# Kernel tuning notes

Measured on AMD Instinct MI355X. Metric: run time of the kernel, lower is better.

The kernel has to match this reference:

```python
import jax, jax.numpy as jnp
import numpy as np

N_NODES = 100000


def gin_layer(x, src, dst, W, b):
    # GINConv with Linear nn, eps=0: Linear(x + sum_{j in N(i)} x_j)
    agg = jax.ops.segment_sum(x[src], dst, num_segments=N_NODES)  # [N, d]
    return (x + agg) @ W + b


def setup_inputs() -> dict:
    key = jax.random.key(0)
    ks = jax.random.split(key, 8)
    in_c, hid, out_c = 128, 128, 64
    x = jax.random.normal(ks[0], (N_NODES, in_c), dtype=jnp.float32)
    edge_index = jax.random.randint(ks[1], (2, 600000), 0, N_NODES, dtype=jnp.int64)
    def lin(k, fan_in, fan_out):
        bound = 1.0 / np.sqrt(fan_in)
        kw, kb = jax.random.split(k)
        W = jax.random.uniform(kw, (fan_in, fan_out), minval=-bound, maxval=bound, dtype=jnp.float32)
        b = jax.random.uniform(kb, (fan_out,), minval=-bound, maxval=bound, dtype=jnp.float32)
        return W, b
    W1, b1 = lin(ks[2], in_c, hid)
    W2, b2 = lin(ks[3], hid, hid)
    W3, b3 = lin(ks[4], hid, out_c)
    return {"x": x, "edge_index": edge_index, "W1": W1, "b1": b1,
            "W2": W2, "b2": b2, "W3": W3, "b3": b3}


def reference(x, edge_index, W1, b1, W2, b2, W3, b3):
    src, dst = edge_index[0], edge_index[1]
    # dropout in eval mode -> identity
    h = jax.nn.relu(gin_layer(x, src, dst, W1, b1))
    h = jax.nn.relu(gin_layer(h, src, dst, W2, b2))
    h = gin_layer(h, src, dst, W3, b3)
    return h
```

## Files before the change

kernel.cpp:

```cpp
#include <hip/hip_runtime.h>


typedef __attribute__((ext_vector_type(8))) short short8;
typedef __attribute__((ext_vector_type(4))) float f32x4;
typedef unsigned short ushort_t;
typedef unsigned int uint_t;

__device__ inline ushort_t bf16_rne(float f) {
  uint_t u = __float_as_uint(f);
  uint_t r = (u + 0x7FFFu + ((u >> 16) & 1u)) >> 16;
  return (ushort_t)r;
}
__device__ inline float bf16_to_f32(ushort_t h) {
  return __uint_as_float(((uint_t)h) << 16);
}

__global__ __launch_bounds__(256) void k_detect(const int* __restrict__ ew,
                                                int* __restrict__ flag, int E) {
  int i = blockIdx.x * 256 + threadIdx.x;
  int idx = 2 * i + 1;
  if (idx < 2 * E) {
    if (ew[idx] != 0) atomicOr(flag, 1);
  }
}

__global__ __launch_bounds__(256) void k_hist(const void* __restrict__ edges,
                                              const int* __restrict__ flag,
                                              int* __restrict__ counts, int E) {
  int e = blockIdx.x * 256 + threadIdx.x;
  if (e >= E) return;
  int d;
  if (*flag) d = ((const int*)edges)[E + e];
  else       d = (int)((const long long*)edges)[E + e];
  atomicAdd(&counts[d], 1);
}

__global__ __launch_bounds__(256) void k_scan1(const int* __restrict__ counts,
                                               int* __restrict__ offs,
                                               int* __restrict__ bsum, int N) {
  __shared__ int s[256];
  int t = threadIdx.x;
  int base = blockIdx.x * 1024 + t * 4;
  int c0 = 0, c1 = 0, c2 = 0, c3 = 0;
  if (base + 0 < N) c0 = counts[base + 0];
  if (base + 1 < N) c1 = counts[base + 1];
  if (base + 2 < N) c2 = counts[base + 2];
  if (base + 3 < N) c3 = counts[base + 3];
  int mySum = c0 + c1 + c2 + c3;
  s[t] = mySum;
  __syncthreads();
  for (int d = 1; d < 256; d <<= 1) {
    int v = (t >= d) ? s[t - d] : 0;
    __syncthreads();
    s[t] += v;
    __syncthreads();
  }
  int excl = s[t] - mySum;
  if (base + 0 < N) offs[base + 0] = excl;
  if (base + 1 < N) offs[base + 1] = excl + c0;
  if (base + 2 < N) offs[base + 2] = excl + c0 + c1;
  if (base + 3 < N) offs[base + 3] = excl + c0 + c1 + c2;
  if (t == 255) bsum[blockIdx.x] = s[255];
}

__global__ __launch_bounds__(128) void k_scan2(int* __restrict__ bsum, int nb) {
  __shared__ int s[128];
  int t = threadIdx.x;
  int v = (t < nb) ? bsum[t] : 0;
  s[t] = v;
  __syncthreads();
  for (int d = 1; d < 128; d <<= 1) {
    int u = (t >= d) ? s[t - d] : 0;
    __syncthreads();
    s[t] += u;
    __syncthreads();
  }
  if (t < nb) bsum[t] = s[t] - v;
}

__global__ __launch_bounds__(256) void k_scan3(int* __restrict__ offs,
                                               const int* __restrict__ bsum,
                                               int* __restrict__ cursor,
                                               int N, int E) {
  int t = threadIdx.x;
  int add = bsum[blockIdx.x];
  int base = blockIdx.x * 1024 + t * 4;
#pragma unroll
  for (int j = 0; j < 4; j++) {
    int i = base + j;
    if (i < N) { int v = offs[i] + add; offs[i] = v; cursor[i] = v; }
  }
  if (blockIdx.x == 0 && t == 0) offs[N] = E;
}

__global__ __launch_bounds__(256) void k_fill(const void* __restrict__ edges,
                                              const int* __restrict__ flag,
                                              int* __restrict__ cursor,
                                              int* __restrict__ csr, int E) {
  int e = blockIdx.x * 256 + threadIdx.x;
  if (e >= E) return;
  int s, d;
  if (*flag) {
    const int* p = (const int*)edges;
    s = p[e]; d = p[E + e];
  } else {
    const long long* p = (const long long*)edges;
    s = (int)p[e]; d = (int)p[E + e];
  }
  int pos = atomicAdd(&cursor[d], 1);
  csr[pos] = s;
}

__global__ __launch_bounds__(256) void k_repack(
    const float* __restrict__ W1, const float* __restrict__ W2,
    const float* __restrict__ W3,
    ushort_t* __restrict__ h1, ushort_t* __restrict__ l1,
    ushort_t* __restrict__ h2, ushort_t* __restrict__ l2,
    ushort_t* __restrict__ h3, ushort_t* __restrict__ l3) {
  int idx = blockIdx.x * 256 + threadIdx.x;
  const float* W; ushort_t* H; ushort_t* L; int NC; int i;
  if (idx < 16384)      { W = W1; H = h1; L = l1; NC = 128; i = idx; }
  else if (idx < 32768) { W = W2; H = h2; L = l2; NC = 128; i = idx - 16384; }
  else if (idx < 40960) { W = W3; H = h3; L = l3; NC = 64;  i = idx - 32768; }
  else return;
  int j = i & 7;
  int lane = (i >> 3) & 63;
  int NT = NC >> 4;
  int tile = (i >> 9) & (NT - 1);
  int ks = i >> (9 + (NC == 128 ? 3 : 2));
  int k = ks * 32 + (lane >> 4) * 8 + j;
  int n = tile * 16 + (lane & 15);
  float v = W[(size_t)k * NC + n];
  ushort_t hi = bf16_rne(v);
  ushort_t lo = bf16_rne(v - bf16_to_f32(hi));
  H[i] = hi; L[i] = lo;
}

template <int NC>
__global__ __launch_bounds__(256) void k_gemm_mfma(
    const float* __restrict__ A, const ushort_t* __restrict__ Bhi,
    const ushort_t* __restrict__ Blo, ushort_t* __restrict__ Z, int M) {
  constexpr int NT = NC / 16;
  int lane = threadIdx.x & 63;
  int wave = threadIdx.x >> 6;
  int row0 = blockIdx.x * 64 + wave * 16;
  int m = lane & 15;
  int q = lane >> 4;
  int grow = row0 + m;
  bool rowok = (grow < M);

  f32x4 acc[NT];
#pragma unroll
  for (int t = 0; t < NT; t++) { acc[t][0] = 0.f; acc[t][1] = 0.f; acc[t][2] = 0.f; acc[t][3] = 0.f; }

  const float* arow = A + (size_t)(rowok ? grow : 0) * 128 + q * 8;

#pragma unroll
  for (int ks = 0; ks < 4; ks++) {
    float av[8];
    *(float4*)(av)     = *(const float4*)(arow + ks * 32);
    *(float4*)(av + 4) = *(const float4*)(arow + ks * 32 + 4);
    short8 ahi, alo;
#pragma unroll
    for (int j = 0; j < 8; j++) {
      float v = av[j];
      ushort_t hi = bf16_rne(v);
      ahi[j] = (short)hi;
      alo[j] = (short)bf16_rne(v - bf16_to_f32(hi));
    }
#pragma unroll
    for (int t = 0; t < NT; t++) {
      const short8 bh = *(const short8*)(Bhi + (((size_t)ks * NT + t) * 64 + lane) * 8);
      const short8 bl = *(const short8*)(Blo + (((size_t)ks * NT + t) * 64 + lane) * 8);
      acc[t] = __builtin_amdgcn_mfma_f32_16x16x32_bf16(ahi, bh, acc[t], 0, 0, 0);
      acc[t] = __builtin_amdgcn_mfma_f32_16x16x32_bf16(ahi, bl, acc[t], 0, 0, 0);
      acc[t] = __builtin_amdgcn_mfma_f32_16x16x32_bf16(alo, bh, acc[t], 0, 0, 0);
    }
  }

  int zrow = row0 + q * 4;
#pragma unroll
  for (int r = 0; r < 4; r++) {
    if (zrow + r < M) {
#pragma unroll
      for (int t = 0; t < NT; t++)
        Z[(size_t)(zrow + r) * NC + t * 16 + m] = bf16_rne(acc[t][r]);
    }
  }
}

template <int NC>
__global__ __launch_bounds__(256, 4) void k_fused(
    const ushort_t* __restrict__ Zin, const int* __restrict__ csr,
    const int* __restrict__ offs, const float* __restrict__ bias,
    const ushort_t* __restrict__ Bhi, const ushort_t* __restrict__ Blo,
    ushort_t* __restrict__ Zout, int M) {
  constexpr int NT = NC / 16;
  int lane = threadIdx.x & 63;
  int wave = threadIdx.x >> 6;
  int row0 = blockIdx.x * 64 + wave * 16;
  int m = lane & 15;
  int q = lane >> 4;
  int grow = row0 + m;
  bool rowok = (grow < M);

  float av[4][8];
  const ushort_t* zr0 = Zin + (size_t)(rowok ? grow : 0) * 128 + q * 8;
  const float* bq = bias + q * 8;
#pragma unroll
  for (int ks = 0; ks < 4; ks++) {
    float4 b0 = *(const float4*)(bq + ks * 32);
    float4 b1 = *(const float4*)(bq + ks * 32 + 4);
    short8 u = *(const short8*)(zr0 + ks * 32);
    av[ks][0] = b0.x + bf16_to_f32((ushort_t)u[0]);
    av[ks][1] = b0.y + bf16_to_f32((ushort_t)u[1]);
    av[ks][2] = b0.z + bf16_to_f32((ushort_t)u[2]);
    av[ks][3] = b0.w + bf16_to_f32((ushort_t)u[3]);
    av[ks][4] = b1.x + bf16_to_f32((ushort_t)u[4]);
    av[ks][5] = b1.y + bf16_to_f32((ushort_t)u[5]);
    av[ks][6] = b1.z + bf16_to_f32((ushort_t)u[6]);
    av[ks][7] = b1.w + bf16_to_f32((ushort_t)u[7]);
  }

  int s = 0, e = 0;
  if (rowok) { s = offs[grow]; e = offs[grow + 1]; }
  int j = s;
  for (; j + 2 <= e; j += 2) {
    int i0 = csr[j], i1 = csr[j + 1];
    const ushort_t* za = Zin + (size_t)i0 * 128 + q * 8;
    const ushort_t* zb = Zin + (size_t)i1 * 128 + q * 8;
    short8 ua[4], ub[4];
#pragma unroll
    for (int ks = 0; ks < 4; ks++) ua[ks] = *(const short8*)(za + ks * 32);
#pragma unroll
    for (int ks = 0; ks < 4; ks++) ub[ks] = *(const short8*)(zb + ks * 32);
#pragma unroll
    for (int ks = 0; ks < 4; ks++)
#pragma unroll
      for (int jj = 0; jj < 8; jj++)
        av[ks][jj] += bf16_to_f32((ushort_t)ua[ks][jj]) +
                      bf16_to_f32((ushort_t)ub[ks][jj]);
  }
  if (j < e) {
    int i0 = csr[j];
    const ushort_t* za = Zin + (size_t)i0 * 128 + q * 8;
#pragma unroll
    for (int ks = 0; ks < 4; ks++) {
      short8 u = *(const short8*)(za + ks * 32);
#pragma unroll
      for (int jj = 0; jj < 8; jj++)
        av[ks][jj] += bf16_to_f32((ushort_t)u[jj]);
    }
  }

  f32x4 acc[NT];
#pragma unroll
  for (int tt = 0; tt < NT; tt++) { acc[tt][0] = 0.f; acc[tt][1] = 0.f; acc[tt][2] = 0.f; acc[tt][3] = 0.f; }

#pragma unroll
  for (int ks = 0; ks < 4; ks++) {
    short8 ahi, alo;
#pragma unroll
    for (int jj = 0; jj < 8; jj++) {
      float v = fmaxf(av[ks][jj], 0.f);
      ushort_t hi = bf16_rne(v);
      ahi[jj] = (short)hi;
      alo[jj] = (short)bf16_rne(v - bf16_to_f32(hi));
    }
#pragma unroll
    for (int tt = 0; tt < NT; tt++) {
      const short8 bh = *(const short8*)(Bhi + (((size_t)ks * NT + tt) * 64 + lane) * 8);
      const short8 bl = *(const short8*)(Blo + (((size_t)ks * NT + tt) * 64 + lane) * 8);
      acc[tt] = __builtin_amdgcn_mfma_f32_16x16x32_bf16(ahi, bh, acc[tt], 0, 0, 0);
      acc[tt] = __builtin_amdgcn_mfma_f32_16x16x32_bf16(ahi, bl, acc[tt], 0, 0, 0);
      acc[tt] = __builtin_amdgcn_mfma_f32_16x16x32_bf16(alo, bh, acc[tt], 0, 0, 0);
    }
  }

  int zrow = row0 + q * 4;
#pragma unroll
  for (int r = 0; r < 4; r++) {
    if (zrow + r < M) {
#pragma unroll
      for (int tt = 0; tt < NT; tt++)
        Zout[(size_t)(zrow + r) * NC + tt * 16 + m] = bf16_rne(acc[tt][r]);
    }
  }
}

__global__ __launch_bounds__(256) void k_agg64(const ushort_t* __restrict__ z,
                                               const int* __restrict__ csr,
                                               const int* __restrict__ offs,
                                               const float* __restrict__ bias,
                                               float* __restrict__ out, int N) {
  int t = threadIdx.x;
  int node = blockIdx.x * 32 + (t >> 3);
  if (node >= N) return;
  int c = (t & 7) * 8;
  float acc[8];
  {
    short8 u = *(const short8*)(z + (size_t)node * 64 + c);
#pragma unroll
    for (int jj = 0; jj < 8; jj++)
      acc[jj] = bias[c + jj] + bf16_to_f32((ushort_t)u[jj]);
  }
  int s = offs[node], e = offs[node + 1];
  int j = s;
  for (; j + 4 <= e; j += 4) {
    int i0 = csr[j], i1 = csr[j + 1], i2 = csr[j + 2], i3 = csr[j + 3];
    short8 u0 = *(const short8*)(z + (size_t)i0 * 64 + c);
    short8 u1 = *(const short8*)(z + (size_t)i1 * 64 + c);
    short8 u2 = *(const short8*)(z + (size_t)i2 * 64 + c);
    short8 u3 = *(const short8*)(z + (size_t)i3 * 64 + c);
#pragma unroll
    for (int jj = 0; jj < 8; jj++)
      acc[jj] += (bf16_to_f32((ushort_t)u0[jj]) + bf16_to_f32((ushort_t)u1[jj])) +
                 (bf16_to_f32((ushort_t)u2[jj]) + bf16_to_f32((ushort_t)u3[jj]));
  }
  for (; j < e; j++) {
    int i0 = csr[j];
    short8 u = *(const short8*)(z + (size_t)i0 * 64 + c);
#pragma unroll
    for (int jj = 0; jj < 8; jj++)
      acc[jj] += bf16_to_f32((ushort_t)u[jj]);
  }
  float4 o0 = make_float4(acc[0], acc[1], acc[2], acc[3]);
  float4 o1 = make_float4(acc[4], acc[5], acc[6], acc[7]);
  *(float4*)&out[(size_t)node * 64 + c]     = o0;
  *(float4*)&out[(size_t)node * 64 + c + 4] = o1;
}

extern "C" void kernel_launch(void* const* d_in, const int* in_sizes, int n_in,
                              void* d_out, int out_size, void* d_ws, size_t ws_size,
                              hipStream_t stream) {
  const float* x  = (const float*)d_in[0];
  const void* edges = d_in[1];
  const float* W1 = (const float*)d_in[2];
  const float* b1 = (const float*)d_in[3];
  const float* W2 = (const float*)d_in[4];
  const float* b2 = (const float*)d_in[5];
  const float* W3 = (const float*)d_in[6];
  const float* b3 = (const float*)d_in[7];
  float* out = (float*)d_out;

  int N = in_sizes[0] / 128;
  int E = in_sizes[1] / 2;

  char* w = (char*)d_ws;
  size_t off = 0;
  auto alloc = [&](size_t bytes) -> void* {
    void* p = w + off;
    off = (off + bytes + 255) & ~(size_t)255;
    return p;
  };
  size_t curBytes = ((size_t)N * 4 + 255) & ~(size_t)255;
  int*   cursor = (int*)alloc(curBytes);
  int*   flag   = (int*)alloc(4);
  int*   csr    = (int*)alloc((size_t)E * 4);
  int*   offs   = (int*)alloc((size_t)(N + 1) * 4);
  int*   bsum   = (int*)alloc(4096);
  ushort_t* h1  = (ushort_t*)alloc(16384 * 2);
  ushort_t* l1  = (ushort_t*)alloc(16384 * 2);
  ushort_t* h2  = (ushort_t*)alloc(16384 * 2);
  ushort_t* l2  = (ushort_t*)alloc(16384 * 2);
  ushort_t* h3  = (ushort_t*)alloc(8192 * 2);
  ushort_t* l3  = (ushort_t*)alloc(8192 * 2);
  ushort_t* z1  = (ushort_t*)alloc((size_t)N * 128 * 2);
  ushort_t* z2  = (ushort_t*)alloc((size_t)N * 128 * 2);
  ushort_t* z3  = z1;

  int ge = (E + 255) / 256;
  int nb = (N + 1023) / 1024;

  hipMemsetAsync(cursor, 0, curBytes + 4, stream);
  k_detect<<<4, 256, 0, stream>>>((const int*)edges, flag, E);
  k_hist<<<ge, 256, 0, stream>>>(edges, flag, cursor, E);
  k_scan1<<<nb, 256, 0, stream>>>(cursor, offs, bsum, N);
  k_scan2<<<1, 128, 0, stream>>>(bsum, nb);
  k_scan3<<<nb, 256, 0, stream>>>(offs, bsum, cursor, N, E);
  k_fill<<<ge, 256, 0, stream>>>(edges, flag, cursor, csr, E);
  k_repack<<<160, 256, 0, stream>>>(W1, W2, W3, h1, l1, h2, l2, h3, l3);

  int gm = (N + 63) / 64;
  k_gemm_mfma<128><<<gm, 256, 0, stream>>>(x, h1, l1, z1, N);
  k_fused<128><<<gm, 256, 0, stream>>>(z1, csr, offs, b1, h2, l2, z2, N);
  k_fused<64><<<gm, 256, 0, stream>>>(z2, csr, offs, b2, h3, l3, z3, N);
  k_agg64<<<(N + 31) / 32, 256, 0, stream>>>(z3, csr, offs, b3, out, N);
}
```

Baseline: 297.7 us.

## Software-pipeline neighbor gathers with register double-buffering and index prefetch

Restructures the CSR aggregation loops in the fused layer kernel and the final 64-wide aggregation kernel so that neighbor row gathers for the next group of four edges are issued before the current group is accumulated, with CSR indices prefetched two iterations ahead. Short-degree rows use a branch-free three-gather path. This aims to hide gather latency with more loads in flight per thread. In exchange it holds many more registers, so the launch bounds drop to two blocks per SM, reducing occupancy, and it may issue redundant loads for clamped indices.

```diff
diff --git a/kernel.cpp b/kernel.cpp
--- a/kernel.cpp
+++ b/kernel.cpp
@@ -13,6 +13,23 @@
 }
 __device__ inline float bf16_to_f32(ushort_t h) {
   return __uint_as_float(((uint_t)h) << 16);
+}
+
+__device__ __forceinline__ void gath4(const ushort_t* Zq, int idx, short8* d) {
+  const ushort_t* p = Zq + (size_t)idx * 128;
+#pragma unroll
+  for (int ks = 0; ks < 4; ks++) d[ks] = *(const short8*)(p + ks * 32);
+}
+__device__ __forceinline__ void acc4(float av[4][8], const short8* d) {
+#pragma unroll
+  for (int ks = 0; ks < 4; ks++)
+#pragma unroll
+    for (int jj = 0; jj < 8; jj++)
+      av[ks][jj] += bf16_to_f32((ushort_t)d[ks][jj]);
+}
+__device__ __forceinline__ void acc8(float* a, short8 u) {
+#pragma unroll
+  for (int jj = 0; jj < 8; jj++) a[jj] += bf16_to_f32((ushort_t)u[jj]);
 }
 
 __global__ __launch_bounds__(256) void k_detect(const int* __restrict__ ew,
@@ -190,7 +207,7 @@
 }
 
 template <int NC>
-__global__ __launch_bounds__(256, 4) void k_fused(
+__global__ __launch_bounds__(256, 2) void k_fused(
     const ushort_t* __restrict__ Zin, const int* __restrict__ csr,
     const int* __restrict__ offs, const float* __restrict__ bias,
     const ushort_t* __restrict__ Bhi, const ushort_t* __restrict__ Blo,
@@ -225,32 +242,42 @@
   int s = 0, e = 0;
   if (rowok) { s = offs[grow]; e = offs[grow + 1]; }
   int j = s;
-  for (; j + 2 <= e; j += 2) {
-    int i0 = csr[j], i1 = csr[j + 1];
-    const ushort_t* za = Zin + (size_t)i0 * 128 + q * 8;
-    const ushort_t* zb = Zin + (size_t)i1 * 128 + q * 8;
-    short8 ua[4], ub[4];
-#pragma unroll
-    for (int ks = 0; ks < 4; ks++) ua[ks] = *(const short8*)(za + ks * 32);
-#pragma unroll
-    for (int ks = 0; ks < 4; ks++) ub[ks] = *(const short8*)(zb + ks * 32);
-#pragma unroll
-    for (int ks = 0; ks < 4; ks++)
-#pragma unroll
-      for (int jj = 0; jj < 8; jj++)
-        av[ks][jj] += bf16_to_f32((ushort_t)ua[ks][jj]) +
-                      bf16_to_f32((ushort_t)ub[ks][jj]);
-  }
-  if (j < e) {
-    int i0 = csr[j];
-    const ushort_t* za = Zin + (size_t)i0 * 128 + q * 8;
-#pragma unroll
-    for (int ks = 0; ks < 4; ks++) {
-      short8 u = *(const short8*)(za + ks * 32);
-#pragma unroll
-      for (int jj = 0; jj < 8; jj++)
-        av[ks][jj] += bf16_to_f32((ushort_t)u[jj]);
-    }
+  const ushort_t* Zq = Zin + q * 8;
+
+  if (e - j >= 4) {
+    int em1 = e - 1;
+    short8 dE[8], dO[8];
+    {
+      int i0 = csr[j], i1 = csr[j + 1], i2 = csr[j + 2], i3 = csr[j + 3];
+      gath4(Zq, i0, dE); gath4(Zq, i1, dE + 4);
+      gath4(Zq, i2, dO); gath4(Zq, i3, dO + 4);
+    }
+    int nE0 = csr[min(j + 4, em1)], nE1 = csr[min(j + 5, em1)];
+    int nO0 = csr[min(j + 6, em1)], nO1 = csr[min(j + 7, em1)];
+    while (j + 4 <= e) {
+      int tE0 = csr[min(j + 8, em1)],  tE1 = csr[min(j + 9, em1)];
+      int tO0 = csr[min(j + 10, em1)], tO1 = csr[min(j + 11, em1)];
+      acc4(av, dE); acc4(av, dE + 4);
+      gath4(Zq, nE0, dE); gath4(Zq, nE1, dE + 4);
+      acc4(av, dO); acc4(av, dO + 4);
+      gath4(Zq, nO0, dO); gath4(Zq, nO1, dO + 4);
+      nE0 = tE0; nE1 = tE1; nO0 = tO0; nO1 = tO1;
+      j += 4;
+    }
+    if (j < e)     acc4(av, dE);
+    if (j + 1 < e) acc4(av, dE + 4);
+    if (j + 2 < e) acc4(av, dO);
+  } else if (j < e) {
+    int em1 = e - 1;
+    int d = e - j;
+    int i0 = csr[j], i1 = csr[min(j + 1, em1)], i2 = csr[min(j + 2, em1)];
+    short8 u0[4], u1[4], u2[4];
+    gath4(Zq, i0, u0);
+    gath4(Zq, i1, u1);
+    gath4(Zq, i2, u2);
+    acc4(av, u0);
+    if (d >= 2) acc4(av, u1);
+    if (d >= 3) acc4(av, u2);
   }
 
   f32x4 acc[NT];
@@ -288,42 +315,65 @@
   }
 }
 
-__global__ __launch_bounds__(256) void k_agg64(const ushort_t* __restrict__ z,
-                                               const int* __restrict__ csr,
-                                               const int* __restrict__ offs,
-                                               const float* __restrict__ bias,
-                                               float* __restrict__ out, int N) {
+__global__ __launch_bounds__(256, 2) void k_agg64(const ushort_t* __restrict__ z,
+                                                  const int* __restrict__ csr,
+                                                  const int* __restrict__ offs,
+                                                  const float* __restrict__ bias,
+                                                  float* __restrict__ out, int N) {
   int t = threadIdx.x;
   int node = blockIdx.x * 32 + (t >> 3);
   if (node >= N) return;
   int c = (t & 7) * 8;
+  const ushort_t* Zc = z + c;
   float acc[8];
   {
-    short8 u = *(const short8*)(z + (size_t)node * 64 + c);
+    short8 u = *(const short8*)(Zc + (size_t)node * 64);
 #pragma unroll
     for (int jj = 0; jj < 8; jj++)
       acc[jj] = bias[c + jj] + bf16_to_f32((ushort_t)u[jj]);
   }
   int s = offs[node], e = offs[node + 1];
   int j = s;
-  for (; j + 4 <= e; j += 4) {
-    int i0 = csr[j], i1 = csr[j + 1], i2 = csr[j + 2], i3 = csr[j + 3];
-    short8 u0 = *(const short8*)(z + (size_t)i0 * 64 + c);
-    short8 u1 = *(const short8*)(z + (size_t)i1 * 64 + c);
-    short8 u2 = *(const short8*)(z + (size_t)i2 * 64 + c);
-    short8 u3 = *(const short8*)(z + (size_t)i3 * 64 + c);
-#pragma unroll
-    for (int jj = 0; jj < 8; jj++)
-      acc[jj] += (bf16_to_f32((ushort_t)u0[jj]) + bf16_to_f32((ushort_t)u1[jj])) +
-                 (bf16_to_f32((ushort_t)u2[jj]) + bf16_to_f32((ushort_t)u3[jj]));
-  }
-  for (; j < e; j++) {
-    int i0 = csr[j];
-    short8 u = *(const short8*)(z + (size_t)i0 * 64 + c);
-#pragma unroll
-    for (int jj = 0; jj < 8; jj++)
-      acc[jj] += bf16_to_f32((ushort_t)u[jj]);
-  }
+
+  if (e - j >= 4) {
+    int em1 = e - 1;
+    short8 dE0, dE1, dO0, dO1;
+    {
+      int i0 = csr[j], i1 = csr[j + 1], i2 = csr[j + 2], i3 = csr[j + 3];
+      dE0 = *(const short8*)(Zc + (size_t)i0 * 64);
+      dE1 = *(const short8*)(Zc + (size_t)i1 * 64);
+      dO0 = *(const short8*)(Zc + (size_t)i2 * 64);
+      dO1 = *(const short8*)(Zc + (size_t)i3 * 64);
+    }
+    int nE0 = csr[min(j + 4, em1)], nE1 = csr[min(j + 5, em1)];
+    int nO0 = csr[min(j + 6, em1)], nO1 = csr[min(j + 7, em1)];
+    while (j + 4 <= e) {
+      int tE0 = csr[min(j + 8, em1)],  tE1 = csr[min(j + 9, em1)];
+      int tO0 = csr[min(j + 10, em1)], tO1 = csr[min(j + 11, em1)];
+      acc8(acc, dE0); acc8(acc, dE1);
+      dE0 = *(const short8*)(Zc + (size_t)nE0 * 64);
+      dE1 = *(const short8*)(Zc + (size_t)nE1 * 64);
+      acc8(acc, dO0); acc8(acc, dO1);
+      dO0 = *(const short8*)(Zc + (size_t)nO0 * 64);
+      dO1 = *(const short8*)(Zc + (size_t)nO1 * 64);
+      nE0 = tE0; nE1 = tE1; nO0 = tO0; nO1 = tO1;
+      j += 4;
+    }
+    if (j < e)     acc8(acc, dE0);
+    if (j + 1 < e) acc8(acc, dE1);
+    if (j + 2 < e) acc8(acc, dO0);
+  } else if (j < e) {
+    int em1 = e - 1;
+    int d = e - j;
+    int i0 = csr[j], i1 = csr[min(j + 1, em1)], i2 = csr[min(j + 2, em1)];
+    short8 u0 = *(const short8*)(Zc + (size_t)i0 * 64);
+    short8 u1 = *(const short8*)(Zc + (size_t)i1 * 64);
+    short8 u2 = *(const short8*)(Zc + (size_t)i2 * 64);
+    acc8(acc, u0);
+    if (d >= 2) acc8(acc, u1);
+    if (d >= 3) acc8(acc, u2);
+  }
+
   float4 o0 = make_float4(acc[0], acc[1], acc[2], acc[3]);
   float4 o1 = make_float4(acc[4], acc[5], acc[6], acc[7]);
   *(float4*)&out[(size_t)node * 64 + c]     = o0;
```

Measured after the change: 320.7 us. 1.08x slower.

## Split neighbor gather across two wave halves with LDS reduction in fused and agg kernels

Applied to the files above, without the earlier changes.

Doubles the block size of the fused aggregate+GEMM kernels and the final aggregation kernel, so each node's edge list is split in half and gathered by two groups of waves. The second half writes its partial sums to shared memory, and the first half adds them before the MFMA or output store. This aims to raise memory-level parallelism and shorten the latency-bound gather chain per node. The cost is a block-wide barrier, extra LDS traffic, idle waves during the GEMM, and possibly lower occupancy from the LDS footprint (about 33KB in k_fused).

```diff
diff --git a/kernel.cpp b/kernel.cpp
--- a/kernel.cpp
+++ b/kernel.cpp
@@ -190,42 +190,58 @@
 }
 
 template <int NC>
-__global__ __launch_bounds__(256, 4) void k_fused(
+__global__ __launch_bounds__(512, 4) void k_fused(
     const ushort_t* __restrict__ Zin, const int* __restrict__ csr,
     const int* __restrict__ offs, const float* __restrict__ bias,
     const ushort_t* __restrict__ Bhi, const ushort_t* __restrict__ Blo,
     ushort_t* __restrict__ Zout, int M) {
   constexpr int NT = NC / 16;
-  int lane = threadIdx.x & 63;
-  int wave = threadIdx.x >> 6;
-  int row0 = blockIdx.x * 64 + wave * 16;
+  constexpr int S = 132;
+  __shared__ float sacc[64 * S];
+
+  int t = threadIdx.x;
+  int lane = t & 63;
+  int wave = t >> 6;
+  int wv = wave & 3;
+  int half = wave >> 2;
+  int row0 = blockIdx.x * 64 + wv * 16;
   int m = lane & 15;
   int q = lane >> 4;
   int grow = row0 + m;
   bool rowok = (grow < M);
 
   float av[4][8];
-  const ushort_t* zr0 = Zin + (size_t)(rowok ? grow : 0) * 128 + q * 8;
-  const float* bq = bias + q * 8;
-#pragma unroll
-  for (int ks = 0; ks < 4; ks++) {
-    float4 b0 = *(const float4*)(bq + ks * 32);
-    float4 b1 = *(const float4*)(bq + ks * 32 + 4);
-    short8 u = *(const short8*)(zr0 + ks * 32);
-    av[ks][0] = b0.x + bf16_to_f32((ushort_t)u[0]);
-    av[ks][1] = b0.y + bf16_to_f32((ushort_t)u[1]);
-    av[ks][2] = b0.z + bf16_to_f32((ushort_t)u[2]);
-    av[ks][3] = b0.w + bf16_to_f32((ushort_t)u[3]);
-    av[ks][4] = b1.x + bf16_to_f32((ushort_t)u[4]);
-    av[ks][5] = b1.y + bf16_to_f32((ushort_t)u[5]);
-    av[ks][6] = b1.z + bf16_to_f32((ushort_t)u[6]);
-    av[ks][7] = b1.w + bf16_to_f32((ushort_t)u[7]);
+  if (half == 0) {
+    const ushort_t* zr0 = Zin + (size_t)(rowok ? grow : 0) * 128 + q * 8;
+    const float* bq = bias + q * 8;
+#pragma unroll
+    for (int ks = 0; ks < 4; ks++) {
+      float4 b0 = *(const float4*)(bq + ks * 32);
+      float4 b1 = *(const float4*)(bq + ks * 32 + 4);
+      short8 u = *(const short8*)(zr0 + ks * 32);
+      av[ks][0] = b0.x + bf16_to_f32((ushort_t)u[0]);
+      av[ks][1] = b0.y + bf16_to_f32((ushort_t)u[1]);
+      av[ks][2] = b0.z + bf16_to_f32((ushort_t)u[2]);
+      av[ks][3] = b0.w + bf16_to_f32((ushort_t)u[3]);
+      av[ks][4] = b1.x + bf16_to_f32((ushort_t)u[4]);
+      av[ks][5] = b1.y + bf16_to_f32((ushort_t)u[5]);
+      av[ks][6] = b1.z + bf16_to_f32((ushort_t)u[6]);
+      av[ks][7] = b1.w + bf16_to_f32((ushort_t)u[7]);
+    }
+  } else {
+#pragma unroll
+    for (int ks = 0; ks < 4; ks++)
+#pragma unroll
+      for (int jj = 0; jj < 8; jj++) av[ks][jj] = 0.f;
   }
 
   int s = 0, e = 0;
   if (rowok) { s = offs[grow]; e = offs[grow + 1]; }
-  int j = s;
-  for (; j + 2 <= e; j += 2) {
+  int mid = (s + e) >> 1;
+  int j  = half ? mid : s;
+  int je = half ? e   : mid;
+
+  for (; j + 2 <= je; j += 2) {
     int i0 = csr[j], i1 = csr[j + 1];
     const ushort_t* za = Zin + (size_t)i0 * 128 + q * 8;
     const ushort_t* zb = Zin + (size_t)i1 * 128 + q * 8;
@@ -241,7 +257,7 @@
         av[ks][jj] += bf16_to_f32((ushort_t)ua[ks][jj]) +
                       bf16_to_f32((ushort_t)ub[ks][jj]);
   }
-  if (j < e) {
+  if (j < je) {
     int i0 = csr[j];
     const ushort_t* za = Zin + (size_t)i0 * 128 + q * 8;
 #pragma unroll
@@ -251,6 +267,28 @@
       for (int jj = 0; jj < 8; jj++)
         av[ks][jj] += bf16_to_f32((ushort_t)u[jj]);
     }
+  }
+
+  if (half) {
+    float* dst = sacc + (wv * 16 + m) * S + q * 8;
+#pragma unroll
+    for (int ks = 0; ks < 4; ks++)
+#pragma unroll
+      for (int jj = 0; jj < 8; jj += 2)
+        *(float2*)(dst + ks * 32 + jj) = make_float2(av[ks][jj], av[ks][jj + 1]);
+  }
+  __syncthreads();
+  if (half) return;
+  {
+    const float* src = sacc + (wv * 16 + m) * S + q * 8;
+#pragma unroll
+    for (int ks = 0; ks < 4; ks++)
+#pragma unroll
+      for (int jj = 0; jj < 8; jj += 2) {
+        float2 p = *(const float2*)(src + ks * 32 + jj);
+        av[ks][jj]     += p.x;
+        av[ks][jj + 1] += p.y;
+      }
   }
 
   f32x4 acc[NT];
@@ -288,46 +326,78 @@
   }
 }
 
-__global__ __launch_bounds__(256) void k_agg64(const ushort_t* __restrict__ z,
-                                               const int* __restrict__ csr,
-                                               const int* __restrict__ offs,
-                                               const float* __restrict__ bias,
-                                               float* __restrict__ out, int N) {
+__global__ __launch_bounds__(512, 4) void k_agg64(const ushort_t* __restrict__ z,
+                                                  const int* __restrict__ csr,
+                                                  const int* __restrict__ offs,
+                                                  const float* __restrict__ bias,
+                                                  float* __restrict__ out, int N) {
+  constexpr int S = 68;
+  __shared__ float sacc[32 * S];
   int t = threadIdx.x;
-  int node = blockIdx.x * 32 + (t >> 3);
-  if (node >= N) return;
-  int c = (t & 7) * 8;
+  int half = t >> 8;
+  int t2 = t & 255;
+  int nl = t2 >> 3;
+  int node = blockIdx.x * 32 + nl;
+  bool nodeok = (node < N);
+  int c = (t2 & 7) * 8;
+
   float acc[8];
-  {
-    short8 u = *(const short8*)(z + (size_t)node * 64 + c);
+  if (half == 0) {
+    short8 u = *(const short8*)(z + (size_t)(nodeok ? node : 0) * 64 + c);
 #pragma unroll
     for (int jj = 0; jj < 8; jj++)
       acc[jj] = bias[c + jj] + bf16_to_f32((ushort_t)u[jj]);
-  }
-  int s = offs[node], e = offs[node + 1];
-  int j = s;
-  for (; j + 4 <= e; j += 4) {
-    int i0 = csr[j], i1 = csr[j + 1], i2 = csr[j + 2], i3 = csr[j + 3];
+  } else {
+#pragma unroll
+    for (int jj = 0; jj < 8; jj++) acc[jj] = 0.f;
+  }
+
+  int s = 0, e = 0;
+  if (nodeok) { s = offs[node]; e = offs[node + 1]; }
+  int mid = (s + e) >> 1;
+  int j  = half ? mid : s;
+  int je = half ? e   : mid;
+
+  for (; j + 2 <= je; j += 2) {
+    int i0 = csr[j], i1 = csr[j + 1];
     short8 u0 = *(const short8*)(z + (size_t)i0 * 64 + c);
     short8 u1 = *(const short8*)(z + (size_t)i1 * 64 + c);
-    short8 u2 = *(const short8*)(z + (size_t)i2 * 64 + c);
-    short8 u3 = *(const short8*)(z + (size_t)i3 * 64 + c);
 #pragma unroll
     for (int jj = 0; jj < 8; jj++)
-      acc[jj] += (bf16_to_f32((ushort_t)u0[jj]) + bf16_to_f32((ushort_t)u1[jj])) +
-                 (bf16_to_f32((ushort_t)u2[jj]) + bf16_to_f32((ushort_t)u3[jj]));
-  }
-  for (; j < e; j++) {
+      acc[jj] += bf16_to_f32((ushort_t)u0[jj]) + bf16_to_f32((ushort_t)u1[jj]);
+  }
+  if (j < je) {
     int i0 = csr[j];
     short8 u = *(const short8*)(z + (size_t)i0 * 64 + c);
 #pragma unroll
     for (int jj = 0; jj < 8; jj++)
       acc[jj] += bf16_to_f32((ushort_t)u[jj]);
   }
-  float4 o0 = make_float4(acc[0], acc[1], acc[2], acc[3]);
-  float4 o1 = make_float4(acc[4], acc[5], acc[6], acc[7]);
-  *(float4*)&out[(size_t)node * 64 + c]     = o0;
-  *(float4*)&out[(size_t)node * 64 + c + 4] = o1;
+
+  if (half) {
+    float* dst = sacc + nl * S + c;
+#pragma unroll
+    for (int jj = 0; jj < 8; jj += 2)
+      *(float2*)(dst + jj) = make_float2(acc[jj], acc[jj + 1]);
+  }
+  __syncthreads();
+  if (half) return;
+  {
+    const float* sp = sacc + nl * S + c;
+#pragma unroll
+    for (int jj = 0; jj < 8; jj += 2) {
+      float2 p = *(const float2*)(sp + jj);
+      acc[jj]     += p.x;
+      acc[jj + 1] += p.y;
+    }
+  }
+
+  if (nodeok) {
+    float4 o0 = make_float4(acc[0], acc[1], acc[2], acc[3]);
+    float4 o1 = make_float4(acc[4], acc[5], acc[6], acc[7]);
+    *(float4*)&out[(size_t)node * 64 + c]     = o0;
+    *(float4*)&out[(size_t)node * 64 + c + 4] = o1;
+  }
 }
 
 extern "C" void kernel_launch(void* const* d_in, const int* in_sizes, int n_in,
@@ -383,7 +453,7 @@
 
   int gm = (N + 63) / 64;
   k_gemm_mfma<128><<<gm, 256, 0, stream>>>(x, h1, l1, z1, N);
-  k_fused<128><<<gm, 256, 0, stream>>>(z1, csr, offs, b1, h2, l2, z2, N);
-  k_fused<64><<<gm, 256, 0, stream>>>(z2, csr, offs, b2, h3, l3, z3, N);
-  k_agg64<<<(N + 31) / 32, 256, 0, stream>>>(z3, csr, offs, b3, out, N);
-}
+  k_fused<128><<<gm, 512, 0, stream>>>(z1, csr, offs, b1, h2, l2, z2, N);
+  k_fused<64><<<gm, 512, 0, stream>>>(z2, csr, offs, b2, h3, l3, z3, N);
+  k_agg64<<<(N + 31) / 32, 512, 0, stream>>>(z3, csr, offs, b3, out, N);
+}
```

Result: slower. 321.7 us (+8.1%).
